# Kernel tuning notes

Hardware: AMD Instinct MI355X
Metric: run time of the kernel (lower is better)

Reference implementation:

```python
import jax, jax.numpy as jnp
import numpy as np

EMB = 2048
N_HEADS = 16
HEAD_DIM = EMB // N_HEADS
ROPE_BASE = 10000.0


def _rope_cos_sin(seq_len, head_dim, dtype):
    inv_freq = 1.0 / (ROPE_BASE ** (jnp.arange(0, head_dim, 2, dtype=jnp.float32) / head_dim))
    t = jnp.arange(seq_len, dtype=jnp.float32)
    freqs = jnp.einsum('s,d->sd', t, inv_freq)          # [S, head_dim/2]
    emb = jnp.concatenate([freqs, freqs], axis=-1)       # [S, head_dim]
    return jnp.cos(emb).astype(dtype), jnp.sin(emb).astype(dtype)


def _rotate_half(x):
    x1, x2 = jnp.split(x, 2, axis=-1)
    return jnp.concatenate([-x2, x1], axis=-1)


def _apply_rope(x, cos, sin):
    # x: [B, H, S, D]; cos/sin: [S, D]
    return x * cos[None, None, :, :] + _rotate_half(x) * sin[None, None, :, :]


def setup_inputs() -> dict:
    key = jax.random.key(0)
    k1, k2, k3 = jax.random.split(key, 3)
    B, S = 4, 2048
    x = jax.random.normal(k1, (B, S, EMB), dtype=jnp.float32)
    # Additive causal mask: 0 on/below diagonal, -1e9 above.
    causal = jnp.triu(jnp.full((S, S), -1e9, dtype=jnp.float32), k=1)
    att_mask = causal[None, None, :, :]
    Wqkv = jax.random.normal(k2, (3 * EMB, EMB), dtype=jnp.float32) * (EMB ** -0.5)
    Wout = jax.random.normal(k3, (EMB, EMB), dtype=jnp.float32) * (EMB ** -0.5)
    return {"x": x, "att_mask": att_mask, "Wqkv": Wqkv, "Wout": Wout}


def reference(x, att_mask, Wqkv, Wout):
    B, S, E = x.shape
    qkv = jnp.einsum('bse,fe->bsf', x, Wqkv)             # [B, S, 3E]
    q, k, v = jnp.split(qkv, 3, axis=-1)
    def to_heads(t):
        return t.reshape(B, S, N_HEADS, HEAD_DIM).transpose(0, 2, 1, 3)  # [B,H,S,D]
    q, k, v = to_heads(q), to_heads(k), to_heads(v)
    cos, sin = _rope_cos_sin(S, HEAD_DIM, x.dtype)
    q = _apply_rope(q, cos, sin)
    k = _apply_rope(k, cos, sin)
    scaling = HEAD_DIM ** -0.5
    dots = jnp.einsum('bhqd,bhkd->bhqk', q, k) * scaling
    dots = dots + att_mask
    attn = jax.nn.softmax(dots, axis=-1)
    out = jnp.einsum('bhqk,bhkd->bhqd', attn, v)         # [B,H,S,D]
    out = out.transpose(0, 2, 1, 3).reshape(B, S, E)
    return jnp.einsum('bse,fe->bsf', out, Wout)
```

## Files before the change

### kernel.cpp

```cpp
#include <hip/hip_runtime.h>
#include <stdint.h>

typedef __attribute__((ext_vector_type(8))) short short8_t;
typedef __attribute__((ext_vector_type(4))) float f32x4;

__device__ __forceinline__ short f2bf(float f) {
  union { float f; uint32_t u; } v; v.f = f;
  uint32_t r = v.u + 0x7FFFu + ((v.u >> 16) & 1u);
  return (short)(r >> 16);
}
__device__ __forceinline__ float bf2f(short s) {
  union { uint32_t u; float f; } v; v.u = ((uint32_t)(uint16_t)s) << 16; return v.f;
}
__device__ __forceinline__ void gld16(const void* g, void* l) {
  __builtin_amdgcn_global_load_lds((const __attribute__((address_space(1))) void*)g,
                                   (__attribute__((address_space(3))) void*)l, 16, 0, 0);
}

__global__ __launch_bounds__(256) void conv3_kernel(const float* __restrict__ x,
                                                    const float* __restrict__ wqkv,
                                                    const float* __restrict__ wout,
                                                    short* __restrict__ xb,
                                                    short* __restrict__ wqb,
                                                    short* __restrict__ woutb) {
  int i = blockIdx.x * 256 + threadIdx.x;
  const int stride = gridDim.x * 256;
  for (; i < 8388608; i += stride) {
    const float4* src;
    short4* dst;
    int j;
    if (i < 4194304) { src = (const float4*)x; dst = (short4*)xb; j = i; }
    else if (i < 7340032) { src = (const float4*)wqkv; dst = (short4*)wqb; j = i - 4194304; }
    else { src = (const float4*)wout; dst = (short4*)woutb; j = i - 7340032; }
    float4 v = src[j];
    short4 o;
    o.x = f2bf(v.x); o.y = f2bf(v.y); o.z = f2bf(v.z); o.w = f2bf(v.w);
    dst[j] = o;
  }
}

__device__ __forceinline__ void storeC(float* C, size_t i, float v) { C[i] = v; }
__device__ __forceinline__ void storeC(short* C, size_t i, float v) { C[i] = f2bf(v); }

template <typename OT, bool FUSEV>
__global__ __launch_bounds__(512, 2) void gemm8p(const short* __restrict__ A,
                                                 const short* __restrict__ B,
                                                 OT* __restrict__ C,
                                                 short* __restrict__ VT,
                                                 int M, int N, int K) {
  __shared__ __align__(16) short lds[65536];
  const int tid = threadIdx.x, lane = tid & 63, w = tid >> 6;
  const int wr = w >> 2, wc = w & 3;
  const int c = lane & 15, g4 = lane >> 4;
  const int xcd = (int)blockIdx.x & 7;
  const int t = (int)blockIdx.x >> 3;
  const int bx = (t & 7) + 8 * (t >> 5);
  const int by = xcd * 4 + ((t >> 3) & 3);
  const size_t m0 = (size_t)by * 256, n0 = (size_t)bx * 256;
  const size_t Kb = (size_t)K * 2;
  const char* Ab = (const char*)A + m0 * Kb;
  const char* Bb = (const char*)B + n0 * Kb;
  const char* aq[2];
  const char* bq[2];
#pragma unroll
  for (int i = 0; i < 2; ++i) {
    const size_t ro = (size_t)((i * 8 + w) * 16 + c) * Kb + g4 * 16;
    aq[i] = Ab + ro;
    bq[i] = Bb + ro;
  }
  char* alds = (char*)lds;
  const int aoff = wr * 8192 + lane * 16;
  const int boff = 65536 + wc * 4096 + lane * 16;
  f32x4 acc[8][4] = {};
  const int NT = K >> 6, NIT = NT >> 1;

  short8_t af[2][4], bfr[2][4];

#define STAGE(q, srcoff, ldsbase)                                  \
  gld16((q)[0] + (srcoff), alds + (ldsbase) + (w << 10));          \
  gld16((q)[1] + (srcoff), alds + (ldsbase) + ((8 + w) << 10))

  STAGE(aq, 0, 0);
  STAGE(bq, 0, 65536);
  STAGE(aq, 64, 16384);
  STAGE(bq, 64, 81920);
  STAGE(aq, 128, 32768);
  STAGE(bq, 128, 98304);
  asm volatile("s_waitcnt vmcnt(0)" ::: "memory");
  asm volatile("s_barrier" ::: "memory");

#define RD_A(S, mi, OFF) \
  asm volatile("ds_read_b128 %0, %1 offset:%c2" : "=v"(af[S][mi]) : "v"(aoff), "i"(OFF))
#define RD_B(S, ni, OFF) \
  asm volatile("ds_read_b128 %0, %1 offset:%c2" : "=v"(bfr[S][ni]) : "v"(boff), "i"(OFF))

#define PREF_A(S, BSEL, KS, MQ)                           \
  RD_A(S, 0, (BSEL) + (KS)*16384 + ((MQ)*4 + 0) * 1024);  \
  RD_A(S, 1, (BSEL) + (KS)*16384 + ((MQ)*4 + 1) * 1024);  \
  RD_A(S, 2, (BSEL) + (KS)*16384 + ((MQ)*4 + 2) * 1024);  \
  RD_A(S, 3, (BSEL) + (KS)*16384 + ((MQ)*4 + 3) * 1024)

#define PREF_B(S, BSEL, KS)                  \
  RD_B(S, 0, (BSEL) + (KS)*16384 + 0);       \
  RD_B(S, 1, (BSEL) + (KS)*16384 + 1024);    \
  RD_B(S, 2, (BSEL) + (KS)*16384 + 2048);    \
  RD_B(S, 3, (BSEL) + (KS)*16384 + 3072)

#define MFMA16(AS, BS, MQ)                                                               \
  __builtin_amdgcn_s_setprio(1);                                                         \
  _Pragma("unroll") for (int mi = 0; mi < 4; ++mi) {                                     \
    _Pragma("unroll") for (int n = 0; n < 4; ++n)                                        \
      acc[(MQ)*4 + mi][n] = __builtin_amdgcn_mfma_f32_16x16x32_bf16(                     \
          af[AS][mi], bfr[BS][n], acc[(MQ)*4 + mi][n], 0, 0, 0);                         \
  }                                                                                      \
  __builtin_amdgcn_s_setprio(0)

#define PHASE_E(AS, BS, PBSEL, PKS, q, srcoff, sbase)              \
  PREF_A(AS ^ 1, PBSEL, PKS, 1);                                   \
  STAGE(q, srcoff, sbase);                                         \
  asm volatile("s_waitcnt lgkmcnt(4)" ::: "memory");               \
  __builtin_amdgcn_sched_barrier(0);                               \
  MFMA16(AS, BS, 0);                                               \
  asm volatile("s_barrier" ::: "memory")

#define PHASE_O(AS, BS, PBSEL, PKS, q, srcoff, sbase, GATE)        \
  PREF_B(BS ^ 1, PBSEL, PKS);                                      \
  PREF_A(AS ^ 1, PBSEL, PKS, 0);                                   \
  STAGE(q, srcoff, sbase);                                         \
  asm volatile("s_waitcnt lgkmcnt(8)" ::: "memory");               \
  __builtin_amdgcn_sched_barrier(0);                               \
  MFMA16(AS, BS, 1);                                               \
  GATE;                                                            \
  asm volatile("s_barrier" ::: "memory")

#define GATE8 asm volatile("s_waitcnt vmcnt(8)" ::: "memory")
#define GATE4 asm volatile("s_waitcnt vmcnt(4)" ::: "memory")
#define NOGATE (void)0

  PREF_B(0, 0, 0);
  PREF_A(0, 0, 0, 0);

  for (int it = 0; it < NIT; ++it) {
    const int T = it << 1;
    const int t1 = (T + 1) << 7;
    const int t2 = (T + 2 < NT ? T + 2 : NT - 1) << 7;
    const int t3 = (T + 3 < NT ? T + 3 : NT - 1) << 7;
    PHASE_E(0, 0, 0, 0,      aq, t1 + 64, 49152);
    PHASE_O(1, 0, 0, 1,      bq, t1 + 64, 114688, NOGATE);
    PHASE_E(0, 1, 0, 1,      aq, t2, 0);
    PHASE_O(1, 1, 32768, 0,  bq, t2, 65536, GATE8);
    PHASE_E(0, 0, 32768, 0,  aq, t2 + 64, 16384);
    PHASE_O(1, 0, 32768, 1,  bq, t2 + 64, 81920, NOGATE);
    PHASE_E(0, 1, 32768, 1,  aq, t3, 32768);
    PHASE_O(1, 1, 0, 0,      bq, t3, 98304, GATE4);
  }
#undef PHASE_E
#undef PHASE_O
#undef GATE8
#undef GATE4
#undef NOGATE
#undef MFMA16
#undef PREF_A
#undef PREF_B
#undef RD_A
#undef RD_B
#undef STAGE

#pragma unroll
  for (int m = 0; m < 8; ++m)
#pragma unroll
    for (int n = 0; n < 4; ++n) {
      const size_t col = n0 + wc * 64 + n * 16 + c;
      const size_t rb = m0 + wr * 128 + m * 16 + g4 * 4;
      bool tovt = false;
      if constexpr (FUSEV) tovt = (col >= 4096);
      if (tovt) {
        const size_t cc = col - 4096;
        const size_t b = rb >> 11, s0 = rb & 2047;
        short4 o;
        o.x = f2bf(acc[m][n][0]); o.y = f2bf(acc[m][n][1]);
        o.z = f2bf(acc[m][n][2]); o.w = f2bf(acc[m][n][3]);
        *(short4*)&VT[(b * 2048 + cc) * 2048 + s0] = o;
      } else {
#pragma unroll
        for (int r = 0; r < 4; ++r) storeC(C, (rb + r) * (size_t)N + col, acc[m][n][r]);
      }
    }
}

__global__ __launch_bounds__(256) void rope_kernel(short* __restrict__ qkv) {
  const int g = blockIdx.x * 256 + threadIdx.x;
  const int jg = g & 7;
  const int h = (g >> 3) & 15;
  const int bs = g >> 7;
  const int s = bs & 2047;
  const size_t base = (size_t)bs * 6144 + 2048 + h * 128 + jg * 8;
  short8_t lo = *(short8_t*)&qkv[base];
  short8_t hi = *(short8_t*)&qkv[base + 64];
  short8_t olo, ohi;
#pragma unroll
  for (int t = 0; t < 8; ++t) {
    const int j = jg * 8 + t;
    const float inv = exp2f((float)j * -0.20762050593046f);
    float sn, cn;
    sincosf((float)s * inv, &sn, &cn);
    const float a = bf2f(lo[t]), b = bf2f(hi[t]);
    olo[t] = f2bf(a * cn - b * sn);
    ohi[t] = f2bf(b * cn + a * sn);
  }
  *(short8_t*)&qkv[base] = olo;
  *(short8_t*)&qkv[base + 64] = ohi;
}

__global__ __launch_bounds__(256) void attn_kernel(const short* __restrict__ qkv,
                                                   const short* __restrict__ vt,
                                                   short* __restrict__ o) {
  __shared__ __align__(16) short Kl[2][32 * 128];
  __shared__ __align__(16) short Vl[2][128 * 32];
  __shared__ __align__(16) short Pl[4][16 * 40];
  const int tid = threadIdx.x, lane = tid & 63, w = tid >> 6;
  const int c = lane & 15, g4 = lane >> 4;
  const int blk = blockIdx.x;
  const int xcd = blk & 7;
  const int l = blk >> 3;
  const int bh = xcd * 8 + (l >> 5);
  const int h = bh & 15, b = bh >> 4;
  const int q0 = (31 - (l & 31)) * 64;
  const int srow = q0 + w * 16 + c;

  short8_t qf[4];
  {
    const size_t qr = ((size_t)b * 2048 + srow) * 6144 + h * 128;
    float fl[4][8];
#pragma unroll
    for (int dc = 0; dc < 4; ++dc) {
      short8_t rawv = *(const short8_t*)&qkv[qr + dc * 32 + g4 * 8];
#pragma unroll
      for (int t = 0; t < 8; ++t) fl[dc][t] = bf2f(rawv[t]);
    }
#pragma unroll
    for (int pd = 0; pd < 2; ++pd)
#pragma unroll
      for (int t = 0; t < 8; ++t) {
        const int j = pd * 32 + g4 * 8 + t;
        const float inv = exp2f((float)j * -0.20762050593046f);
        float sn, cn;
        sincosf((float)srow * inv, &sn, &cn);
        const float a = fl[pd][t], bb = fl[pd + 2][t];
        fl[pd][t] = a * cn - bb * sn;
        fl[pd + 2][t] = bb * cn + a * sn;
      }
#pragma unroll
    for (int dc = 0; dc < 4; ++dc) {
      short8_t q8;
#pragma unroll
      for (int t = 0; t < 8; ++t) q8[t] = f2bf(fl[dc][t]);
      qf[dc] = q8;
    }
  }

  f32x4 acc_o[8] = {};
  float rs[4] = {0.f, 0.f, 0.f, 0.f};
  const float scale2 = 0.12751875222364685f;
  const char* Kbase = (const char*)qkv + ((size_t)b * 2048 * 6144 + 2048 + h * 128) * 2;
  const char* Vbase = (const char*)vt + ((size_t)(b * 16 + h) * 128 * 2048) * 2;

  const char* kq[2];
  const char* vq[2];
#pragma unroll
  for (int i = 0; i < 2; ++i) {
    const int L = ((w * 2 + i) << 10) + lane * 16;
    {
      const int row = L >> 8, inner = L & 255;
      kq[i] = Kbase + (size_t)row * 12288 + (inner ^ ((row & 7) << 4));
    }
    {
      const int row = L >> 6, inner = L & 63;
      vq[i] = Vbase + (size_t)row * 4096 + (inner ^ ((row & 3) << 4));
    }
  }
  auto stage = [&](int buf, int kv0) {
#pragma unroll
    for (int i = 0; i < 2; ++i) {
      gld16(kq[i] + (size_t)kv0 * 12288, (char*)Kl + (buf << 13) + ((w * 2 + i) << 10));
      gld16(vq[i] + (size_t)kv0 * 2, (char*)Vl + (buf << 13) + ((w * 2 + i) << 10));
    }
  };

  stage(0, 0);
  __syncthreads();
  int cur = 0;
  const int kvend = q0 + 32;
  for (int kv0 = 0; kv0 <= kvend; kv0 += 32) {
    if (kv0 <= q0) stage(cur ^ 1, kv0 + 32);
    const char* Kb = (const char*)Kl + (cur << 13);
    const char* Vb = (const char*)Vl + (cur << 13);
    const bool diag = (kv0 >= q0);
    float p[2][4];
#pragma unroll
    for (int kt = 0; kt < 2; ++kt) {
      f32x4 s4 = {};
      const int krow = kt * 16 + c;
      __builtin_amdgcn_s_setprio(1);
#pragma unroll
      for (int dc = 0; dc < 4; ++dc) {
        const int inner = (dc * 64 + g4 * 16) ^ ((krow & 7) << 4);
        short8_t kf = *(const short8_t*)(Kb + krow * 256 + inner);
        s4 = __builtin_amdgcn_mfma_f32_16x16x32_bf16(qf[dc], kf, s4, 0, 0, 0);
      }
      __builtin_amdgcn_s_setprio(0);
#pragma unroll
      for (int r = 0; r < 4; ++r) {
        float v = s4[r] * scale2 - 8.0f;
        if (diag) {
          const int kc = kv0 + kt * 16 + c;
          const int qr2 = q0 + w * 16 + g4 * 4 + r;
          if (kc > qr2) v = -1e30f;
        }
        const float pe = exp2f(v);
        p[kt][r] = pe;
        rs[r] += pe;
      }
    }
#pragma unroll
    for (int kt = 0; kt < 2; ++kt)
#pragma unroll
      for (int r = 0; r < 4; r += 2) {
        uint32_t pk;
        asm("v_cvt_pk_bf16_f32 %0, %1, %2" : "=v"(pk) : "v"(p[kt][r]), "v"(p[kt][r + 1]));
        Pl[w][(g4 * 4 + r) * 40 + kt * 16 + c] = (short)(pk & 0xffffu);
        Pl[w][(g4 * 4 + r + 1) * 40 + kt * 16 + c] = (short)(pk >> 16);
      }
    {
      short8_t pf = *(const short8_t*)&Pl[w][c * 40 + g4 * 8];
      __builtin_amdgcn_s_setprio(1);
#pragma unroll
      for (int dt = 0; dt < 8; ++dt) {
        const int vrow = dt * 16 + c;
        const int inner = (g4 * 16) ^ ((vrow & 3) << 4);
        short8_t vf = *(const short8_t*)(Vb + vrow * 64 + inner);
        acc_o[dt] = __builtin_amdgcn_mfma_f32_16x16x32_bf16(pf, vf, acc_o[dt], 0, 0, 0);
      }
      __builtin_amdgcn_s_setprio(0);
    }
    __syncthreads();
    cur ^= 1;
  }
#pragma unroll
  for (int off = 1; off < 16; off <<= 1)
#pragma unroll
    for (int r = 0; r < 4; ++r) rs[r] += __shfl_xor(rs[r], off);
  const size_t ob = ((size_t)b * 2048 + q0 + w * 16 + g4 * 4) * 2048 + h * 128;
#pragma unroll
  for (int dt = 0; dt < 8; ++dt)
#pragma unroll
    for (int r = 0; r < 4; ++r)
      o[ob + (size_t)r * 2048 + dt * 16 + c] = f2bf(acc_o[dt][r] / rs[r]);
}

extern "C" void kernel_launch(void* const* d_in, const int* in_sizes, int n_in,
                              void* d_out, int out_size, void* d_ws, size_t ws_size,
                              hipStream_t stream) {
  const float* x = (const float*)d_in[0];
  const float* Wqkv = (const float*)d_in[2];
  const float* Wout = (const float*)d_in[3];
  float* out = (float*)d_out;
  char* ws = (char*)d_ws;
  short* xb   = (short*)ws;
  short* wqb  = (short*)(ws + 33554432ull);
  short* qkv  = (short*)(ws + 58720256ull);
  short* vt   = (short*)(ws + 159383552ull);
  short* attno = xb;
  short* woutb = wqb + 6291456;
  woutb = (short*)(ws + 192937984ull);

  conv3_kernel<<<2048, 256, 0, stream>>>(x, Wqkv, Wout, xb, wqb, woutb);
  gemm8p<short, true><<<768, 512, 0, stream>>>(xb, wqb, qkv, vt, 8192, 6144, 2048);
  rope_kernel<<<4096, 256, 0, stream>>>(qkv);
  attn_kernel<<<2048, 256, 0, stream>>>(qkv, vt, attno);
  gemm8p<float, false><<<256, 512, 0, stream>>>(attno, woutb, out, nullptr, 8192, 2048, 2048);
}
```

Before: 503.9 us.

## Double query rows per attention block to reuse K/V tiles across two row groups

Each attention workgroup now handles 128 query rows instead of 64, with every wave holding two 16-row query fragments. K fragments are loaded from LDS once and reused for both row groups, and each V fragment feeds two MFMAs, which halves LDS and global K/V traffic per query. The grid shrinks to 1024 blocks and per-wave register use roughly doubles for the accumulators. The causal diagonal region grows, so the masked tiles that still get computed increase, and occupancy may drop.

```diff
diff --git a/kernel.cpp b/kernel.cpp
--- a/kernel.cpp
+++ b/kernel.cpp
@@ -217,19 +217,20 @@
                                                    short* __restrict__ o) {
   __shared__ __align__(16) short Kl[2][32 * 128];
   __shared__ __align__(16) short Vl[2][128 * 32];
-  __shared__ __align__(16) short Pl[4][16 * 40];
+  __shared__ __align__(16) short Pl[4][32 * 40];
   const int tid = threadIdx.x, lane = tid & 63, w = tid >> 6;
   const int c = lane & 15, g4 = lane >> 4;
   const int blk = blockIdx.x;
   const int xcd = blk & 7;
   const int l = blk >> 3;
-  const int bh = xcd * 8 + (l >> 5);
+  const int bh = xcd * 8 + (l >> 4);
   const int h = bh & 15, b = bh >> 4;
-  const int q0 = (31 - (l & 31)) * 64;
-  const int srow = q0 + w * 16 + c;
-
-  short8_t qf[4];
-  {
+  const int q0 = (15 - (l & 15)) * 128;
+
+  short8_t qf[2][4];
+#pragma unroll
+  for (int rg = 0; rg < 2; ++rg) {
+    const int srow = q0 + w * 32 + rg * 16 + c;
     const size_t qr = ((size_t)b * 2048 + srow) * 6144 + h * 128;
     float fl[4][8];
 #pragma unroll
@@ -255,12 +256,12 @@
       short8_t q8;
 #pragma unroll
       for (int t = 0; t < 8; ++t) q8[t] = f2bf(fl[dc][t]);
-      qf[dc] = q8;
-    }
-  }
-
-  f32x4 acc_o[8] = {};
-  float rs[4] = {0.f, 0.f, 0.f, 0.f};
+      qf[rg][dc] = q8;
+    }
+  }
+
+  f32x4 acc_o[2][8] = {};
+  float rs[2][4] = {};
   const float scale2 = 0.12751875222364685f;
   const char* Kbase = (const char*)qkv + ((size_t)b * 2048 * 6144 + 2048 + h * 128) * 2;
   const char* Vbase = (const char*)vt + ((size_t)(b * 16 + h) * 128 * 2048) * 2;
@@ -290,72 +291,91 @@
   stage(0, 0);
   __syncthreads();
   int cur = 0;
-  const int kvend = q0 + 32;
+  const int kvend = q0 + 96;
   for (int kv0 = 0; kv0 <= kvend; kv0 += 32) {
-    if (kv0 <= q0) stage(cur ^ 1, kv0 + 32);
+    if (kv0 + 32 <= kvend) stage(cur ^ 1, kv0 + 32);
     const char* Kb = (const char*)Kl + (cur << 13);
     const char* Vb = (const char*)Vl + (cur << 13);
-    const bool diag = (kv0 >= q0);
-    float p[2][4];
+    const bool diag = (kv0 >= q0 + w * 32);
+    short8_t kf[2][4];
 #pragma unroll
     for (int kt = 0; kt < 2; ++kt) {
-      f32x4 s4 = {};
       const int krow = kt * 16 + c;
-      __builtin_amdgcn_s_setprio(1);
 #pragma unroll
       for (int dc = 0; dc < 4; ++dc) {
         const int inner = (dc * 64 + g4 * 16) ^ ((krow & 7) << 4);
-        short8_t kf = *(const short8_t*)(Kb + krow * 256 + inner);
-        s4 = __builtin_amdgcn_mfma_f32_16x16x32_bf16(qf[dc], kf, s4, 0, 0, 0);
+        kf[kt][dc] = *(const short8_t*)(Kb + krow * 256 + inner);
       }
-      __builtin_amdgcn_s_setprio(0);
-#pragma unroll
-      for (int r = 0; r < 4; ++r) {
-        float v = s4[r] * scale2 - 8.0f;
-        if (diag) {
-          const int kc = kv0 + kt * 16 + c;
-          const int qr2 = q0 + w * 16 + g4 * 4 + r;
-          if (kc > qr2) v = -1e30f;
+    }
+    float p[2][2][4];
+#pragma unroll
+    for (int rg = 0; rg < 2; ++rg) {
+#pragma unroll
+      for (int kt = 0; kt < 2; ++kt) {
+        f32x4 s4 = {};
+        __builtin_amdgcn_s_setprio(1);
+#pragma unroll
+        for (int dc = 0; dc < 4; ++dc)
+          s4 = __builtin_amdgcn_mfma_f32_16x16x32_bf16(qf[rg][dc], kf[kt][dc], s4, 0, 0, 0);
+        __builtin_amdgcn_s_setprio(0);
+#pragma unroll
+        for (int r = 0; r < 4; ++r) {
+          float v = s4[r] * scale2 - 8.0f;
+          if (diag) {
+            const int kc = kv0 + kt * 16 + c;
+            const int qr2 = q0 + w * 32 + rg * 16 + g4 * 4 + r;
+            if (kc > qr2) v = -1e30f;
+          }
+          const float pe = exp2f(v);
+          p[rg][kt][r] = pe;
+          rs[rg][r] += pe;
         }
-        const float pe = exp2f(v);
-        p[kt][r] = pe;
-        rs[r] += pe;
       }
     }
 #pragma unroll
-    for (int kt = 0; kt < 2; ++kt)
-#pragma unroll
-      for (int r = 0; r < 4; r += 2) {
-        uint32_t pk;
-        asm("v_cvt_pk_bf16_f32 %0, %1, %2" : "=v"(pk) : "v"(p[kt][r]), "v"(p[kt][r + 1]));
-        Pl[w][(g4 * 4 + r) * 40 + kt * 16 + c] = (short)(pk & 0xffffu);
-        Pl[w][(g4 * 4 + r + 1) * 40 + kt * 16 + c] = (short)(pk >> 16);
-      }
-    {
-      short8_t pf = *(const short8_t*)&Pl[w][c * 40 + g4 * 8];
-      __builtin_amdgcn_s_setprio(1);
-#pragma unroll
-      for (int dt = 0; dt < 8; ++dt) {
-        const int vrow = dt * 16 + c;
-        const int inner = (g4 * 16) ^ ((vrow & 3) << 4);
-        short8_t vf = *(const short8_t*)(Vb + vrow * 64 + inner);
-        acc_o[dt] = __builtin_amdgcn_mfma_f32_16x16x32_bf16(pf, vf, acc_o[dt], 0, 0, 0);
-      }
-      __builtin_amdgcn_s_setprio(0);
-    }
+    for (int rg = 0; rg < 2; ++rg)
+#pragma unroll
+      for (int kt = 0; kt < 2; ++kt)
+#pragma unroll
+        for (int r = 0; r < 4; r += 2) {
+          uint32_t pk;
+          asm("v_cvt_pk_bf16_f32 %0, %1, %2"
+              : "=v"(pk) : "v"(p[rg][kt][r]), "v"(p[rg][kt][r + 1]));
+          Pl[w][(rg * 16 + g4 * 4 + r) * 40 + kt * 16 + c] = (short)(pk & 0xffffu);
+          Pl[w][(rg * 16 + g4 * 4 + r + 1) * 40 + kt * 16 + c] = (short)(pk >> 16);
+        }
+    short8_t pf[2];
+#pragma unroll
+    for (int rg = 0; rg < 2; ++rg)
+      pf[rg] = *(const short8_t*)&Pl[w][(rg * 16 + c) * 40 + g4 * 8];
+    __builtin_amdgcn_s_setprio(1);
+#pragma unroll
+    for (int dt = 0; dt < 8; ++dt) {
+      const int vrow = dt * 16 + c;
+      const int inner = (g4 * 16) ^ ((vrow & 3) << 4);
+      const short8_t vf = *(const short8_t*)(Vb + vrow * 64 + inner);
+      acc_o[0][dt] = __builtin_amdgcn_mfma_f32_16x16x32_bf16(pf[0], vf, acc_o[0][dt], 0, 0, 0);
+      acc_o[1][dt] = __builtin_amdgcn_mfma_f32_16x16x32_bf16(pf[1], vf, acc_o[1][dt], 0, 0, 0);
+    }
+    __builtin_amdgcn_s_setprio(0);
     __syncthreads();
     cur ^= 1;
   }
 #pragma unroll
   for (int off = 1; off < 16; off <<= 1)
 #pragma unroll
-    for (int r = 0; r < 4; ++r) rs[r] += __shfl_xor(rs[r], off);
-  const size_t ob = ((size_t)b * 2048 + q0 + w * 16 + g4 * 4) * 2048 + h * 128;
-#pragma unroll
-  for (int dt = 0; dt < 8; ++dt)
-#pragma unroll
-    for (int r = 0; r < 4; ++r)
-      o[ob + (size_t)r * 2048 + dt * 16 + c] = f2bf(acc_o[dt][r] / rs[r]);
+    for (int rg = 0; rg < 2; ++rg)
+#pragma unroll
+      for (int r = 0; r < 4; ++r) rs[rg][r] += __shfl_xor(rs[rg][r], off);
+#pragma unroll
+  for (int rg = 0; rg < 2; ++rg) {
+    const size_t ob = ((size_t)b * 2048 + q0 + w * 32 + rg * 16 + g4 * 4) * 2048 + h * 128;
+#pragma unroll
+    for (int dt = 0; dt < 8; ++dt)
+#pragma unroll
+      for (int r = 0; r < 4; ++r)
+        o[ob + (size_t)r * 2048 + dt * 16 + c] = f2bf(acc_o[rg][dt][r] / rs[rg][r]);
+  }
 }
 
 extern "C" void kernel_launch(void* const* d_in, const int* in_sizes, int n_in,
@@ -366,17 +386,16 @@
   const float* Wout = (const float*)d_in[3];
   float* out = (float*)d_out;
   char* ws = (char*)d_ws;
-  short* xb   = (short*)ws;
-  short* wqb  = (short*)(ws + 33554432ull);
-  short* qkv  = (short*)(ws + 58720256ull);
-  short* vt   = (short*)(ws + 159383552ull);
+  short* xb    = (short*)ws;
+  short* wqb   = (short*)(ws + 33554432ull);
+  short* qkv   = (short*)(ws + 58720256ull);
+  short* vt    = (short*)(ws + 159383552ull);
+  short* woutb = (short*)(ws + 192937984ull);
   short* attno = xb;
-  short* woutb = wqb + 6291456;
-  woutb = (short*)(ws + 192937984ull);
 
   conv3_kernel<<<2048, 256, 0, stream>>>(x, Wqkv, Wout, xb, wqb, woutb);
   gemm8p<short, true><<<768, 512, 0, stream>>>(xb, wqb, qkv, vt, 8192, 6144, 2048);
   rope_kernel<<<4096, 256, 0, stream>>>(qkv);
-  attn_kernel<<<2048, 256, 0, stream>>>(qkv, vt, attno);
+  attn_kernel<<<1024, 256, 0, stream>>>(qkv, vt, attno);
   gemm8p<float, false><<<256, 512, 0, stream>>>(attno, woutb, out, nullptr, 8192, 2048, 2048);
 }
```

Result: slower. 533.5 us (+5.9%).
